# Kernel tuning notes

Hardware: AMD Instinct MI355X
Metric: run time of the kernel (lower is better)

Reference implementation:

```python
import jax, jax.numpy as jnp
import numpy as np

N_NODES = 50000
N_EDGES = 800000
N_TRAIN = 40000
IN_DIM = 129  # node_dim + encoding_dim


def _gatv2(x, src, dst, Wl, Wr, att, bias, heads, out_ch, n_nodes):
    """PyG GATv2Conv (share_weights=False, concat=True, aggr='mean', eval mode).
    x: [N, F_in]; src/dst: [E]; Wl/Wr: [F_in, heads*out_ch]; att: [heads, out_ch]."""
    xl = (x @ Wl).reshape(-1, heads, out_ch)          # source transform  [N,H,C]
    xr = (x @ Wr).reshape(-1, heads, out_ch)          # target transform  [N,H,C]
    e = jax.nn.leaky_relu(xl[src] + xr[dst], 0.2)     # [E,H,C]
    logits = jnp.einsum('ehc,hc->eh', e, att)         # [E,H]
    # segment softmax over incoming edges of each target node
    m = jax.ops.segment_max(logits, dst, num_segments=n_nodes)   # [N,H]
    a = jnp.exp(logits - m[dst])
    denom = jax.ops.segment_sum(a, dst, num_segments=n_nodes)    # [N,H]
    alpha = a / denom[dst]                                       # [E,H]
    msg = xl[src] * alpha[:, :, None]                            # [E,H,C]
    summed = jax.ops.segment_sum(msg, dst, num_segments=n_nodes) # [N,H,C]
    deg = jax.ops.segment_sum(jnp.ones((src.shape[0],), x.dtype), dst,
                              num_segments=n_nodes)              # aggr='mean'
    out = summed / jnp.maximum(deg, 1.0)[:, None, None]
    return out.reshape(n_nodes, heads * out_ch) + bias


def setup_inputs() -> dict:
    key = jax.random.key(0)
    ks = jax.random.split(key, 16)
    x = jax.random.normal(ks[0], (N_NODES, IN_DIM), jnp.float32)
    edge_index = jax.random.randint(ks[1], (2, N_EDGES), 0, N_NODES, jnp.int64)
    y = jax.random.uniform(ks[2], (N_NODES,), jnp.float32)
    train_idx = jnp.sort(jax.random.randint(ks[3], (N_TRAIN,), 0, N_NODES, jnp.int64))

    def lin(k, fi, fo):
        return jax.random.normal(k, (fi, fo), jnp.float32) * (1.0 / np.sqrt(fi))

    return {
        'x': x, 'edge_index': edge_index, 'y': y, 'train_idx': train_idx,
        # layer 1: 129 -> 128, heads=2 (concat -> 256)
        'W1l': lin(ks[4], IN_DIM, 256), 'W1r': lin(ks[5], IN_DIM, 256),
        'a1': jax.random.normal(ks[6], (2, 128), jnp.float32) * 0.1,
        'b1': jnp.zeros((256,), jnp.float32),
        # layer 2: 256 -> 128, heads=1
        'W2l': lin(ks[7], 256, 128), 'W2r': lin(ks[8], 256, 128),
        'a2': jax.random.normal(ks[9], (1, 128), jnp.float32) * 0.1,
        'b2': jnp.zeros((128,), jnp.float32),
        # layer 3: 128 -> 1, heads=1
        'W3l': lin(ks[10], 128, 1), 'W3r': lin(ks[11], 128, 1),
        'a3': jax.random.normal(ks[12], (1, 1), jnp.float32) * 0.1,
        'b3': jnp.zeros((1,), jnp.float32),
    }


def reference(x, edge_index, y, train_idx,
              W1l, W1r, a1, b1, W2l, W2r, a2, b2, W3l, W3r, a3, b3):
    src, dst = edge_index[0], edge_index[1]
    n = x.shape[0]
    h = _gatv2(x, src, dst, W1l, W1r, a1, b1, 2, 128, n)   # [N,256]
    h = _gatv2(h, src, dst, W2l, W2r, a2, b2, 1, 128, n)   # [N,128]
    h = _gatv2(h, src, dst, W3l, W3r, a3, b3, 1, 1, n)     # [N,1]
    pred = jax.nn.sigmoid(h.squeeze(-1))                   # [N]
    return pred[train_idx], y[train_idx]
```

## Files before the change

### kernel.cpp

```cpp
#include <hip/hip_runtime.h>
#include <cmath>

typedef __attribute__((ext_vector_type(2))) float v2f;

__device__ __forceinline__ float lo16(unsigned u){ union{unsigned x; float f;} c; c.x = u << 16; return c.f; }
__device__ __forceinline__ float hi16(unsigned u){ union{unsigned x; float f;} c; c.x = u & 0xffff0000u; return c.f; }
__device__ __forceinline__ float leaky(float v){ return fmaxf(v, 0.2f*v); }
__device__ __forceinline__ v2f pkmax(v2f a, v2f b){ v2f r; r.x = fmaxf(a.x,b.x); r.y = fmaxf(a.y,b.y); return r; }
__device__ __forceinline__ v2f mkv2(unsigned u){ v2f r; r.x = lo16(u); r.y = hi16(u); return r; }
__device__ __forceinline__ unsigned short f2bf(float f){
  union { float f; unsigned u; } c; c.f = f;
  unsigned u = c.u + 0x7FFFu + ((c.u >> 16) & 1u);
  return (unsigned short)(u >> 16);
}
__device__ __forceinline__ unsigned pack2bf(float a, float b){
  return (unsigned)f2bf(a) | ((unsigned)f2bf(b) << 16);
}
__device__ __forceinline__ float mergef(float m, float M){ return (m == M) ? 1.f : __expf(m - M); }

#define LOG2E 1.4426950408889634f

typedef __attribute__((ext_vector_type(8))) short bfrag;
typedef __attribute__((ext_vector_type(4))) float ffrag;


__global__ void deg_kernel(const int* __restrict__ dst, int* __restrict__ degi, int E){
  int e = blockIdx.x*256 + threadIdx.x;
  if (e < E) atomicAdd(&degi[dst[e]], 1);
}

__global__ void scan_p1(const int* __restrict__ degi, int* __restrict__ bsum, int N){
  __shared__ int red[256];
  int t = threadIdx.x;
  int i = blockIdx.x*256 + t;
  red[t] = (i < N) ? degi[i] : 0;
  __syncthreads();
  for (int off = 128; off > 0; off >>= 1){
    if (t < off) red[t] += red[t + off];
    __syncthreads();
  }
  if (t == 0) bsum[blockIdx.x] = red[0];
}

__global__ void scan_p2(const int* __restrict__ bsum, int* __restrict__ boff,
                        int* __restrict__ row_off, int NB, int N){
  __shared__ int s[256];
  int t = threadIdx.x;
  int v = (t < NB) ? bsum[t] : 0;
  s[t] = v;
  __syncthreads();
  for (int off = 1; off < 256; off <<= 1){
    int q = (t >= off) ? s[t - off] : 0;
    __syncthreads();
    s[t] += q;
    __syncthreads();
  }
  if (t < NB) boff[t] = s[t] - v;
  if (t == NB-1) row_off[N] = s[t];
}

__global__ void scan_p3(const int* __restrict__ degi, const int* __restrict__ boff,
                        int* __restrict__ row_off, int* __restrict__ cur, int N){
  __shared__ int s[256];
  int t = threadIdx.x;
  int i = blockIdx.x*256 + t;
  int v = (i < N) ? degi[i] : 0;
  s[t] = v;
  __syncthreads();
  for (int off = 1; off < 256; off <<= 1){
    int q = (t >= off) ? s[t - off] : 0;
    __syncthreads();
    s[t] += q;
    __syncthreads();
  }
  if (i < N){
    int ro = boff[blockIdx.x] + s[t] - v;
    row_off[i] = ro;
    cur[i] = ro;
  }
}

__global__ void scatter_kernel(const int* __restrict__ src, const int* __restrict__ dst,
                               int* __restrict__ cur, int* __restrict__ csr_src, int E){
  int e = blockIdx.x*256 + threadIdx.x;
  if (e < E){
    int pos = atomicAdd(&cur[dst[e]], 1);
    csr_src[pos] = src[e];
  }
}


__global__ void prep_all(const float* __restrict__ x,
                         const float* __restrict__ W1l, const float* __restrict__ W1r,
                         const float* __restrict__ W2l, const float* __restrict__ W2r,
                         unsigned short* __restrict__ Xbf,
                         unsigned short* __restrict__ WT1,
                         unsigned short* __restrict__ WT2, int N){
  int idx = blockIdx.x*256 + threadIdx.x;
  int n1 = N*160;
  int n2 = 2*256*160;
  int n3 = 2*128*256;
  if (idx < n1){
    int n = idx / 160, k = idx - n*160;
    Xbf[idx] = (k < 129) ? f2bf(x[(size_t)n*129 + k]) : (unsigned short)0;
  } else if (idx < n1 + n2){
    int j = idx - n1;
    int c = j / 160, k = j - c*160;
    float v = 0.f;
    if (k < 129) v = (c < 256) ? W1l[(size_t)k*256 + c] : W1r[(size_t)k*256 + (c - 256)];
    WT1[j] = f2bf(v);
  } else if (idx < n1 + n2 + n3){
    int j = idx - n1 - n2;
    int c = j >> 8, k = j & 255;
    float v = (c < 128) ? W2l[(size_t)k*128 + c] : W2r[(size_t)k*128 + (c - 128)];
    WT2[j] = f2bf(v);
  }
}


template<int CB>
__global__ __launch_bounds__(256) void gemm_dual(const unsigned short* __restrict__ Xbf,
                                                 const unsigned short* __restrict__ WT,
                                                 unsigned short* __restrict__ outL,
                                                 unsigned short* __restrict__ outR,
                                                 int N, int Kpad, int Mhalf){
  __shared__ __attribute__((aligned(16))) unsigned short Xs[128*40];
  __shared__ __attribute__((aligned(16))) unsigned short Ws[CB*128*40];
  int t = threadIdx.x;
  int n0 = blockIdx.x*128, c0 = blockIdx.y*(CB*128);
  int wv = t >> 6, lane = t & 63;
  int wr = wv >> 1, wc = wv & 1;
  int m16 = lane & 15, quad = lane >> 4;

  ffrag acc[CB][4][4];
  #pragma unroll
  for (int cb = 0; cb < CB; cb++)
    #pragma unroll
    for (int i = 0; i < 4; i++)
      #pragma unroll
      for (int j = 0; j < 4; j++) acc[cb][i][j] = (ffrag){0.f,0.f,0.f,0.f};

  for (int k0 = 0; k0 < Kpad; k0 += 32){
    uint4 zero = {0,0,0,0};
    #pragma unroll
    for (int it = 0; it < 2; it++){
      int idx = t + it*256;
      int r = idx >> 2, g = idx & 3;
      int n = n0 + r;
      uint4 v = (n < N) ? *(const uint4*)&Xbf[(size_t)n*Kpad + k0 + g*8] : zero;
      *(uint4*)&Xs[r*40 + g*8] = v;
    }
    #pragma unroll
    for (int it = 0; it < 2*CB; it++){
      int idx = t + it*256;
      int c = idx >> 2, g = idx & 3;
      uint4 v = *(const uint4*)&WT[(size_t)(c0 + c)*Kpad + k0 + g*8];
      *(uint4*)&Ws[c*40 + g*8] = v;
    }
    __syncthreads();
    bfrag a[4];
    #pragma unroll
    for (int i = 0; i < 4; i++)
      a[i] = *(const bfrag*)&Xs[(wr*64 + i*16 + m16)*40 + quad*8];
    #pragma unroll
    for (int cb = 0; cb < CB; cb++){
      bfrag b[4];
      #pragma unroll
      for (int j = 0; j < 4; j++)
        b[j] = *(const bfrag*)&Ws[(cb*128 + wc*64 + j*16 + m16)*40 + quad*8];
      #pragma unroll
      for (int i = 0; i < 4; i++)
        #pragma unroll
        for (int j = 0; j < 4; j++)
          acc[cb][i][j] = __builtin_amdgcn_mfma_f32_16x16x32_bf16(a[i], b[j], acc[cb][i][j], 0, 0, 0);
    }
    __syncthreads();
  }

  #pragma unroll
  for (int cb = 0; cb < CB; cb++){
    int gc0 = c0 + cb*128;
    bool isL = (gc0 < Mhalf);
    unsigned short* outp = isL ? outL : outR;
    int ccol0 = isL ? gc0 : (gc0 - Mhalf);
    #pragma unroll
    for (int i = 0; i < 4; i++){
      #pragma unroll
      for (int reg = 0; reg < 4; reg++){
        int rr = n0 + wr*64 + i*16 + quad*4 + reg;
        if (rr >= N) continue;
        #pragma unroll
        for (int j = 0; j < 4; j++){
          int cc = ccol0 + wc*64 + j*16 + m16;
          outp[(size_t)rr*Mhalf + cc] = f2bf(acc[cb][i][j][reg]);
        }
      }
    }
  }
}


__global__ __launch_bounds__(256) void fused_gat_wave2(
    const int* __restrict__ row_off, const int* __restrict__ csr_src,
    const unsigned short* __restrict__ xlbf, const unsigned short* __restrict__ xrbf,
    const float* __restrict__ att, const float* __restrict__ bias,
    unsigned short* __restrict__ outbf, int N)
{
  int n = blockIdx.x*4 + (threadIdx.x >> 6);
  if (n >= N) return;
  int lane = threadIdx.x & 63;
  int slot = lane >> 5;
  int sub  = lane & 31;
  int ch0  = sub*8;
  int r0 = row_off[n], r1 = row_off[n+1];
  int deg = r1 - r0;

  uint4 xru = *(const uint4*)&xrbf[(size_t)n*256 + ch0];
  v2f q01 = mkv2(xru.x), q23 = mkv2(xru.y), q45 = mkv2(xru.z), q67 = mkv2(xru.w);
  const v2f* atp = (const v2f*)(att + ch0);
  v2f at01 = atp[0], at23 = atp[1], at45 = atp[2], at67 = atp[3];

  float m = -INFINITY, l = 0.f;
  v2f A01 = {0.f,0.f}, A23 = {0.f,0.f}, A45 = {0.f,0.f}, A67 = {0.f,0.f};

  if (deg > 0){
    int p = r0 + slot;
    int pc = min(p, r1-1);
    uint4 cur = *(const uint4*)&xlbf[(size_t)csr_src[pc]*256 + ch0];
    for (; p < r1; p += 2){
      int pn = min(p+2, r1-1);
      uint4 nxt = *(const uint4*)&xlbf[(size_t)csr_src[pn]*256 + ch0];
      v2f x01 = mkv2(cur.x), x23 = mkv2(cur.y), x45 = mkv2(cur.z), x67 = mkv2(cur.w);
      v2f t01 = x01 + q01, t23 = x23 + q23, t45 = x45 + q45, t67 = x67 + q67;
      v2f dv = pkmax(t01, t01*0.2f)*at01;
      dv += pkmax(t23, t23*0.2f)*at23;
      dv += pkmax(t45, t45*0.2f)*at45;
      dv += pkmax(t67, t67*0.2f)*at67;
      float dot = dv.x + dv.y;
      dot += __shfl_xor(dot, 8);
      dot += __shfl_xor(dot, 4);
      dot += __shfl_xor(dot, 2);
      dot += __shfl_xor(dot, 1);
      if (dot <= m){
        float w_ = __expf(dot - m);
        l += w_;
        A01 += x01*w_; A23 += x23*w_; A45 += x45*w_; A67 += x67*w_;
      } else {
        float sc = __expf(m - dot);
        l = l*sc + 1.f;
        A01 = A01*sc + x01; A23 = A23*sc + x23; A45 = A45*sc + x45; A67 = A67*sc + x67;
        m = dot;
      }
      cur = nxt;
    }
  }

  const float4* bvp = (const float4*)(bias + ch0);
  float4 res0 = bvp[0], res1 = bvp[1];
  if (deg > 0){
    float m2 = __shfl_xor(m, 32);
    float l2 = __shfl_xor(l, 32);
    float M  = fmaxf(m, m2);
    float fa = mergef(m, M), fb = mergef(m2, M);
    float L  = l*fa + l2*fb;
    v2f q;
    q.x = __shfl_xor(A01.x,32); q.y = __shfl_xor(A01.y,32); A01 = A01*fa + q*fb;
    q.x = __shfl_xor(A23.x,32); q.y = __shfl_xor(A23.y,32); A23 = A23*fa + q*fb;
    q.x = __shfl_xor(A45.x,32); q.y = __shfl_xor(A45.y,32); A45 = A45*fa + q*fb;
    q.x = __shfl_xor(A67.x,32); q.y = __shfl_xor(A67.y,32); A67 = A67*fa + q*fb;
    float inv = 1.f / (L * (float)deg);
    res0.x += A01.x*inv; res0.y += A01.y*inv; res0.z += A23.x*inv; res0.w += A23.y*inv;
    res1.x += A45.x*inv; res1.y += A45.y*inv; res1.z += A67.x*inv; res1.w += A67.y*inv;
  }
  if (slot == 0){
    uint4 u;
    u.x = pack2bf(res0.x, res0.y);
    u.y = pack2bf(res0.z, res0.w);
    u.z = pack2bf(res1.x, res1.y);
    u.w = pack2bf(res1.z, res1.w);
    *(uint4*)&outbf[(size_t)n*256 + ch0] = u;
  }
}


__global__ __launch_bounds__(256) void fused_gat_wave1(
    const int* __restrict__ row_off, const int* __restrict__ csr_src,
    const unsigned short* __restrict__ xlbf, const unsigned short* __restrict__ xrbf,
    const float* __restrict__ att, const float* __restrict__ bias,
    const float* __restrict__ W3l, const float* __restrict__ W3r,
    float* __restrict__ xl3, float* __restrict__ xr3, int N)
{
  int n = blockIdx.x*4 + (threadIdx.x >> 6);
  if (n >= N) return;
  int lane = threadIdx.x & 63;
  int slot = lane >> 4;
  int sub  = lane & 15;
  int ch0  = sub*8;
  int r0 = row_off[n], r1 = row_off[n+1];
  int deg = r1 - r0;

  uint4 xru = *(const uint4*)&xrbf[(size_t)n*128 + ch0];
  v2f q01 = mkv2(xru.x), q23 = mkv2(xru.y), q45 = mkv2(xru.z), q67 = mkv2(xru.w);
  const v2f* atp = (const v2f*)(att + ch0);
  v2f at01 = atp[0], at23 = atp[1], at45 = atp[2], at67 = atp[3];

  float m = -INFINITY, l = 0.f;
  v2f A01 = {0.f,0.f}, A23 = {0.f,0.f}, A45 = {0.f,0.f}, A67 = {0.f,0.f};

  if (deg > 0){
    int p = r0 + slot;
    int pc = min(p, r1-1);
    uint4 cur = *(const uint4*)&xlbf[(size_t)csr_src[pc]*128 + ch0];
    for (; p < r1; p += 4){
      int pn = min(p+4, r1-1);
      uint4 nxt = *(const uint4*)&xlbf[(size_t)csr_src[pn]*128 + ch0];
      v2f x01 = mkv2(cur.x), x23 = mkv2(cur.y), x45 = mkv2(cur.z), x67 = mkv2(cur.w);
      v2f t01 = x01 + q01, t23 = x23 + q23, t45 = x45 + q45, t67 = x67 + q67;
      v2f dv = pkmax(t01, t01*0.2f)*at01;
      dv += pkmax(t23, t23*0.2f)*at23;
      dv += pkmax(t45, t45*0.2f)*at45;
      dv += pkmax(t67, t67*0.2f)*at67;
      float dot = dv.x + dv.y;
      dot += __shfl_xor(dot, 8);
      dot += __shfl_xor(dot, 4);
      dot += __shfl_xor(dot, 2);
      dot += __shfl_xor(dot, 1);
      if (dot <= m){
        float w_ = __expf(dot - m);
        l += w_;
        A01 += x01*w_; A23 += x23*w_; A45 += x45*w_; A67 += x67*w_;
      } else {
        float sc = __expf(m - dot);
        l = l*sc + 1.f;
        A01 = A01*sc + x01; A23 = A23*sc + x23; A45 = A45*sc + x45; A67 = A67*sc + x67;
        m = dot;
      }
      cur = nxt;
    }
  }

  if (deg > 0){
    #pragma unroll
    for (int stage = 0; stage < 2; stage++){
      int d = 16 << stage;
      float m2 = __shfl_xor(m, d);
      float l2 = __shfl_xor(l, d);
      float M  = fmaxf(m, m2);
      float fa = mergef(m, M), fb = mergef(m2, M);
      l = l*fa + l2*fb;
      v2f q;
      q.x = __shfl_xor(A01.x,d); q.y = __shfl_xor(A01.y,d); A01 = A01*fa + q*fb;
      q.x = __shfl_xor(A23.x,d); q.y = __shfl_xor(A23.y,d); A23 = A23*fa + q*fb;
      q.x = __shfl_xor(A45.x,d); q.y = __shfl_xor(A45.y,d); A45 = A45*fa + q*fb;
      q.x = __shfl_xor(A67.x,d); q.y = __shfl_xor(A67.y,d); A67 = A67*fa + q*fb;
      m = M;
    }
  }
  float inv = (deg > 0) ? 1.f/(l*(float)deg) : 0.f;
  const float4* bvp = (const float4*)(bias + ch0);
  float4 res0 = bvp[0], res1 = bvp[1];
  res0.x += A01.x*inv; res0.y += A01.y*inv; res0.z += A23.x*inv; res0.w += A23.y*inv;
  res1.x += A45.x*inv; res1.y += A45.y*inv; res1.z += A67.x*inv; res1.w += A67.y*inv;

  float4 wla = *(const float4*)(W3l + ch0);
  float4 wlb = *(const float4*)(W3l + ch0 + 4);
  float4 wra = *(const float4*)(W3r + ch0);
  float4 wrb = *(const float4*)(W3r + ch0 + 4);
  float sl = res0.x*wla.x + res0.y*wla.y + res0.z*wla.z + res0.w*wla.w
           + res1.x*wlb.x + res1.y*wlb.y + res1.z*wlb.z + res1.w*wlb.w;
  float sr = res0.x*wra.x + res0.y*wra.y + res0.z*wra.z + res0.w*wra.w
           + res1.x*wrb.x + res1.y*wrb.y + res1.z*wrb.z + res1.w*wrb.w;
  sl += __shfl_xor(sl, 8); sl += __shfl_xor(sl, 4); sl += __shfl_xor(sl, 2); sl += __shfl_xor(sl, 1);
  sr += __shfl_xor(sr, 8); sr += __shfl_xor(sr, 4); sr += __shfl_xor(sr, 2); sr += __shfl_xor(sr, 1);
  if (lane == 0){ xl3[n] = sl; xr3[n] = sr; }
}


__global__ __launch_bounds__(256) void aggr3_wave(
    const int* __restrict__ row_off, const int* __restrict__ csr_src,
    const float* __restrict__ xl3, const float* __restrict__ xr3,
    const float* __restrict__ a3, const float* __restrict__ b3,
    float* __restrict__ h3, int N)
{
  int n = blockIdx.x*4 + (threadIdx.x >> 6);
  if (n >= N) return;
  int lane = threadIdx.x & 63;
  int r0 = row_off[n], r1 = row_off[n+1];
  int deg = r1 - r0;
  float b = b3[0];
  if (deg == 0){ if (lane == 0) h3[n] = b; return; }
  float xrv = xr3[n];
  float aa = a3[0] * LOG2E;
  float m = -INFINITY, den = 0.f, s = 0.f;
  for (int base = r0; base < r1; base += 64){
    int p = base + lane;
    bool valid = p < r1;
    float xlv = valid ? xl3[csr_src[p]] : 0.f;
    float t = xlv + xrv;
    float v = fmaxf(t, 0.2f*t) * aa;
    if (!valid) v = -INFINITY;
    float bm = v;
    #pragma unroll
    for (int off = 32; off > 0; off >>= 1) bm = fmaxf(bm, __shfl_xor(bm, off));
    float nm = fmaxf(m, bm);
    float a = valid ? exp2f(v - nm) : 0.f;
    float bd = a, bs = a * xlv;
    #pragma unroll
    for (int off = 32; off > 0; off >>= 1){
      bd += __shfl_xor(bd, off);
      bs += __shfl_xor(bs, off);
    }
    float sc = exp2f(m - nm);
    den = den*sc + bd;
    s   = s*sc + bs;
    m = nm;
  }
  if (lane == 0) h3[n] = s/den/(float)deg + b;
}

__global__ void out_kernel(const float* __restrict__ h3, const float* __restrict__ y,
                           const int* __restrict__ tidx, float* __restrict__ out, int T){
  int i = blockIdx.x*256 + threadIdx.x;
  if (i >= T) return;
  int n = tidx[i];
  out[i] = 1.f/(1.f + __expf(-h3[n]));
  out[T + i] = y[n];
}


extern "C" void kernel_launch(void* const* d_in, const int* in_sizes, int n_in,
                              void* d_out, int out_size, void* d_ws, size_t ws_size,
                              hipStream_t stream){
  const float* x    = (const float*)d_in[0];
  const int*   ei   = (const int*)d_in[1];
  const float* y    = (const float*)d_in[2];
  const int*   tidx = (const int*)d_in[3];
  const float* W1l  = (const float*)d_in[4];
  const float* W1r  = (const float*)d_in[5];
  const float* a1   = (const float*)d_in[6];
  const float* b1   = (const float*)d_in[7];
  const float* W2l  = (const float*)d_in[8];
  const float* W2r  = (const float*)d_in[9];
  const float* a2   = (const float*)d_in[10];
  const float* b2   = (const float*)d_in[11];
  const float* W3l  = (const float*)d_in[12];
  const float* W3r  = (const float*)d_in[13];
  const float* a3   = (const float*)d_in[14];
  const float* b3   = (const float*)d_in[15];

  int N = in_sizes[2];
  int E = in_sizes[1] / 2;
  int T = in_sizes[3];
  const int* src = ei;
  const int* dst = ei + E;
  int NB = (N + 255) / 256;

  char* w = (char*)d_ws;
  size_t off = 0;
  auto take = [&](size_t bytes) -> char* {
    char* p = w + off;
    off = (off + bytes + 255) & ~(size_t)255;
    return p;
  };
  int*   row_off = (int*)  take((size_t)(N+1)*4);
  int*   degi    = (int*)  take((size_t)N*4);
  int*   cur     = (int*)  take((size_t)N*4);
  int*   bsum    = (int*)  take((size_t)NB*4);
  int*   boff    = (int*)  take((size_t)NB*4);
  int*   csr_src = (int*)  take((size_t)E*4);
  unsigned short* WT1 = (unsigned short*)take((size_t)512*160*2);
  unsigned short* WT2 = (unsigned short*)take((size_t)256*256*2);
  float* A       = (float*)take((size_t)N*256*4);
  float* B       = (float*)take((size_t)N*256*4);

  hipMemsetAsync(degi, 0, (size_t)N*4, stream);
  deg_kernel<<<(E+255)/256, 256, 0, stream>>>(dst, degi, E);
  scan_p1<<<NB, 256, 0, stream>>>(degi, bsum, N);
  scan_p2<<<1, 256, 0, stream>>>(bsum, boff, row_off, NB, N);
  scan_p3<<<NB, 256, 0, stream>>>(degi, boff, row_off, cur, N);
  scatter_kernel<<<(E+255)/256, 256, 0, stream>>>(src, dst, cur, csr_src, E);

  unsigned short* xl1bf = (unsigned short*)A;
  unsigned short* Xbf   = (unsigned short*)(A + (size_t)N*128);
  unsigned short* h1bf  = (unsigned short*)(A + (size_t)N*128);
  unsigned short* xr1bf = (unsigned short*)B;
  float* Bu   = B + (size_t)N*128;
  float* xl3  = Bu;
  float* xr3  = Bu + N;
  float* h3   = Bu + 2*(size_t)N;

  int prep_total = N*160 + 2*256*160 + 2*128*256;
  prep_all<<<(prep_total+255)/256, 256, 0, stream>>>(x, W1l, W1r, W2l, W2r, Xbf, WT1, WT2, N);

  gemm_dual<2><<<dim3((N+127)/128, 2), 256, 0, stream>>>(Xbf, WT1, xl1bf, xr1bf, N, 160, 256);
  fused_gat_wave2<<<(N+3)/4, 256, 0, stream>>>(row_off, csr_src, xl1bf, xr1bf, a1, b1, h1bf, N);

  unsigned short* xl2bf = (unsigned short*)A;
  unsigned short* xr2bf = (unsigned short*)B;
  gemm_dual<2><<<dim3((N+127)/128, 1), 256, 0, stream>>>(h1bf, WT2, xl2bf, xr2bf, N, 256, 128);
  fused_gat_wave1<<<(N+3)/4, 256, 0, stream>>>(row_off, csr_src, xl2bf, xr2bf, a2, b2,
                                               W3l, W3r, xl3, xr3, N);

  aggr3_wave<<<(N+3)/4, 256, 0, stream>>>(row_off, csr_src, xl3, xr3, a3, b3, h3, N);

  out_kernel<<<(T+255)/256, 256, 0, stream>>>(h3, y, tidx, (float*)d_out, T);
}
```

Baseline: 392.2 us.

## Merge CSR build and prep into one cooperative kernel; fuse layer-3 aggregation with output

Replaces the memset, degree count, three scan passes, scatter and input/weight conversion kernels with a single cooperative kernel that uses grid-wide syncs between phases. The final-layer aggregation now runs only for training-index nodes and writes the sigmoid and label output directly, which removes the separate output kernel and skips aggregation for nodes that are never read. This cuts launch count and per-launch gaps. In exchange, the CSR and prep phases run on a fixed 1024-block grid with grid barriers, which may lower parallelism compared with the original full-size launches.

```diff
diff --git a/kernel.cpp b/kernel.cpp
--- a/kernel.cpp
+++ b/kernel.cpp
@@ -1,11 +1,13 @@
 #include <hip/hip_runtime.h>
+#include <hip/hip_cooperative_groups.h>
 #include <cmath>
+
+namespace cg = cooperative_groups;
 
 typedef __attribute__((ext_vector_type(2))) float v2f;
 
 __device__ __forceinline__ float lo16(unsigned u){ union{unsigned x; float f;} c; c.x = u << 16; return c.f; }
 __device__ __forceinline__ float hi16(unsigned u){ union{unsigned x; float f;} c; c.x = u & 0xffff0000u; return c.f; }
-__device__ __forceinline__ float leaky(float v){ return fmaxf(v, 0.2f*v); }
 __device__ __forceinline__ v2f pkmax(v2f a, v2f b){ v2f r; r.x = fmaxf(a.x,b.x); r.y = fmaxf(a.y,b.y); return r; }
 __device__ __forceinline__ v2f mkv2(unsigned u){ v2f r; r.x = lo16(u); r.y = hi16(u); return r; }
 __device__ __forceinline__ unsigned short f2bf(float f){
@@ -24,96 +26,105 @@
 typedef __attribute__((ext_vector_type(4))) float ffrag;
 
 
-__global__ void deg_kernel(const int* __restrict__ dst, int* __restrict__ degi, int E){
-  int e = blockIdx.x*256 + threadIdx.x;
-  if (e < E) atomicAdd(&degi[dst[e]], 1);
-}
-
-__global__ void scan_p1(const int* __restrict__ degi, int* __restrict__ bsum, int N){
-  __shared__ int red[256];
-  int t = threadIdx.x;
-  int i = blockIdx.x*256 + t;
-  red[t] = (i < N) ? degi[i] : 0;
-  __syncthreads();
-  for (int off = 128; off > 0; off >>= 1){
-    if (t < off) red[t] += red[t + off];
-    __syncthreads();
-  }
-  if (t == 0) bsum[blockIdx.x] = red[0];
-}
-
-__global__ void scan_p2(const int* __restrict__ bsum, int* __restrict__ boff,
-                        int* __restrict__ row_off, int NB, int N){
+#define CSR_GRID 1024
+
+__global__ __launch_bounds__(256) void csr_prep_kernel(
+    const int* __restrict__ src, const int* __restrict__ dst,
+    int* __restrict__ degi, int* __restrict__ bsum, int* __restrict__ boff,
+    int* __restrict__ row_off, int* __restrict__ cur, int* __restrict__ csr_src,
+    const float* __restrict__ x,
+    const float* __restrict__ W1l, const float* __restrict__ W1r,
+    const float* __restrict__ W2l, const float* __restrict__ W2r,
+    unsigned short* __restrict__ Xbf, unsigned short* __restrict__ WT1,
+    unsigned short* __restrict__ WT2,
+    int N, int E, int NB)
+{
+  cg::grid_group grid = cg::this_grid();
   __shared__ int s[256];
   int t = threadIdx.x;
-  int v = (t < NB) ? bsum[t] : 0;
-  s[t] = v;
-  __syncthreads();
-  for (int off = 1; off < 256; off <<= 1){
-    int q = (t >= off) ? s[t - off] : 0;
-    __syncthreads();
-    s[t] += q;
-    __syncthreads();
-  }
-  if (t < NB) boff[t] = s[t] - v;
-  if (t == NB-1) row_off[N] = s[t];
-}
-
-__global__ void scan_p3(const int* __restrict__ degi, const int* __restrict__ boff,
-                        int* __restrict__ row_off, int* __restrict__ cur, int N){
-  __shared__ int s[256];
-  int t = threadIdx.x;
-  int i = blockIdx.x*256 + t;
-  int v = (i < N) ? degi[i] : 0;
-  s[t] = v;
-  __syncthreads();
-  for (int off = 1; off < 256; off <<= 1){
-    int q = (t >= off) ? s[t - off] : 0;
-    __syncthreads();
-    s[t] += q;
-    __syncthreads();
-  }
-  if (i < N){
-    int ro = boff[blockIdx.x] + s[t] - v;
-    row_off[i] = ro;
-    cur[i] = ro;
-  }
-}
-
-__global__ void scatter_kernel(const int* __restrict__ src, const int* __restrict__ dst,
-                               int* __restrict__ cur, int* __restrict__ csr_src, int E){
-  int e = blockIdx.x*256 + threadIdx.x;
-  if (e < E){
+  int gtid = blockIdx.x*256 + t;
+  int gsize = gridDim.x*256;
+
+  for (int i = gtid; i < N; i += gsize) degi[i] = 0;
+  {
+    int n1 = N*160;
+    int n2 = 2*256*160;
+    int n3 = 2*128*256;
+    int total = n1 + n2 + n3;
+    for (int idx = gtid; idx < total; idx += gsize){
+      if (idx < n1){
+        int n = idx / 160, k = idx - n*160;
+        Xbf[idx] = (k < 129) ? f2bf(x[(size_t)n*129 + k]) : (unsigned short)0;
+      } else if (idx < n1 + n2){
+        int j = idx - n1;
+        int c = j / 160, k = j - c*160;
+        float v = 0.f;
+        if (k < 129) v = (c < 256) ? W1l[(size_t)k*256 + c] : W1r[(size_t)k*256 + (c - 256)];
+        WT1[j] = f2bf(v);
+      } else {
+        int j = idx - n1 - n2;
+        int c = j >> 8, k = j & 255;
+        float v = (c < 128) ? W2l[(size_t)k*128 + c] : W2r[(size_t)k*128 + (c - 128)];
+        WT2[j] = f2bf(v);
+      }
+    }
+  }
+  grid.sync();
+
+  for (int e = gtid; e < E; e += gsize) atomicAdd(&degi[dst[e]], 1);
+  grid.sync();
+
+  for (int chunk = blockIdx.x; chunk < NB; chunk += gridDim.x){
+    int i = chunk*256 + t;
+    s[t] = (i < N) ? degi[i] : 0;
+    __syncthreads();
+    for (int off = 128; off > 0; off >>= 1){
+      if (t < off) s[t] += s[t + off];
+      __syncthreads();
+    }
+    if (t == 0) bsum[chunk] = s[0];
+    __syncthreads();
+  }
+  grid.sync();
+
+  if (blockIdx.x == 0){
+    int v = (t < NB) ? bsum[t] : 0;
+    s[t] = v;
+    __syncthreads();
+    for (int off = 1; off < 256; off <<= 1){
+      int q = (t >= off) ? s[t - off] : 0;
+      __syncthreads();
+      s[t] += q;
+      __syncthreads();
+    }
+    if (t < NB) boff[t] = s[t] - v;
+    if (t == NB-1) row_off[N] = s[t];
+  }
+  grid.sync();
+
+  for (int chunk = blockIdx.x; chunk < NB; chunk += gridDim.x){
+    int i = chunk*256 + t;
+    int v = (i < N) ? degi[i] : 0;
+    s[t] = v;
+    __syncthreads();
+    for (int off = 1; off < 256; off <<= 1){
+      int q = (t >= off) ? s[t - off] : 0;
+      __syncthreads();
+      s[t] += q;
+      __syncthreads();
+    }
+    if (i < N){
+      int ro = boff[chunk] + s[t] - v;
+      row_off[i] = ro;
+      cur[i] = ro;
+    }
+    __syncthreads();
+  }
+  grid.sync();
+
+  for (int e = gtid; e < E; e += gsize){
     int pos = atomicAdd(&cur[dst[e]], 1);
     csr_src[pos] = src[e];
-  }
-}
-
-
-__global__ void prep_all(const float* __restrict__ x,
-                         const float* __restrict__ W1l, const float* __restrict__ W1r,
-                         const float* __restrict__ W2l, const float* __restrict__ W2r,
-                         unsigned short* __restrict__ Xbf,
-                         unsigned short* __restrict__ WT1,
-                         unsigned short* __restrict__ WT2, int N){
-  int idx = blockIdx.x*256 + threadIdx.x;
-  int n1 = N*160;
-  int n2 = 2*256*160;
-  int n3 = 2*128*256;
-  if (idx < n1){
-    int n = idx / 160, k = idx - n*160;
-    Xbf[idx] = (k < 129) ? f2bf(x[(size_t)n*129 + k]) : (unsigned short)0;
-  } else if (idx < n1 + n2){
-    int j = idx - n1;
-    int c = j / 160, k = j - c*160;
-    float v = 0.f;
-    if (k < 129) v = (c < 256) ? W1l[(size_t)k*256 + c] : W1r[(size_t)k*256 + (c - 256)];
-    WT1[j] = f2bf(v);
-  } else if (idx < n1 + n2 + n3){
-    int j = idx - n1 - n2;
-    int c = j >> 8, k = j & 255;
-    float v = (c < 128) ? W2l[(size_t)k*128 + c] : W2r[(size_t)k*128 + (c - 128)];
-    WT2[j] = f2bf(v);
   }
 }
 
@@ -376,55 +387,56 @@
 }
 
 
-__global__ __launch_bounds__(256) void aggr3_wave(
+__global__ __launch_bounds__(256) void aggr3out_wave(
     const int* __restrict__ row_off, const int* __restrict__ csr_src,
     const float* __restrict__ xl3, const float* __restrict__ xr3,
     const float* __restrict__ a3, const float* __restrict__ b3,
-    float* __restrict__ h3, int N)
+    const float* __restrict__ y, const int* __restrict__ tidx,
+    float* __restrict__ out, int T)
 {
-  int n = blockIdx.x*4 + (threadIdx.x >> 6);
-  if (n >= N) return;
+  int i = blockIdx.x*4 + (threadIdx.x >> 6);
+  if (i >= T) return;
   int lane = threadIdx.x & 63;
+  int n = tidx[i];
   int r0 = row_off[n], r1 = row_off[n+1];
   int deg = r1 - r0;
   float b = b3[0];
-  if (deg == 0){ if (lane == 0) h3[n] = b; return; }
-  float xrv = xr3[n];
-  float aa = a3[0] * LOG2E;
-  float m = -INFINITY, den = 0.f, s = 0.f;
-  for (int base = r0; base < r1; base += 64){
-    int p = base + lane;
-    bool valid = p < r1;
-    float xlv = valid ? xl3[csr_src[p]] : 0.f;
-    float t = xlv + xrv;
-    float v = fmaxf(t, 0.2f*t) * aa;
-    if (!valid) v = -INFINITY;
-    float bm = v;
-    #pragma unroll
-    for (int off = 32; off > 0; off >>= 1) bm = fmaxf(bm, __shfl_xor(bm, off));
-    float nm = fmaxf(m, bm);
-    float a = valid ? exp2f(v - nm) : 0.f;
-    float bd = a, bs = a * xlv;
-    #pragma unroll
-    for (int off = 32; off > 0; off >>= 1){
-      bd += __shfl_xor(bd, off);
-      bs += __shfl_xor(bs, off);
-    }
-    float sc = exp2f(m - nm);
-    den = den*sc + bd;
-    s   = s*sc + bs;
-    m = nm;
-  }
-  if (lane == 0) h3[n] = s/den/(float)deg + b;
-}
-
-__global__ void out_kernel(const float* __restrict__ h3, const float* __restrict__ y,
-                           const int* __restrict__ tidx, float* __restrict__ out, int T){
-  int i = blockIdx.x*256 + threadIdx.x;
-  if (i >= T) return;
-  int n = tidx[i];
-  out[i] = 1.f/(1.f + __expf(-h3[n]));
-  out[T + i] = y[n];
+  float h;
+  if (deg == 0){
+    h = b;
+  } else {
+    float xrv = xr3[n];
+    float aa = a3[0] * LOG2E;
+    float m = -INFINITY, den = 0.f, s = 0.f;
+    for (int base = r0; base < r1; base += 64){
+      int p = base + lane;
+      bool valid = p < r1;
+      float xlv = valid ? xl3[csr_src[p]] : 0.f;
+      float t = xlv + xrv;
+      float v = fmaxf(t, 0.2f*t) * aa;
+      if (!valid) v = -INFINITY;
+      float bm = v;
+      #pragma unroll
+      for (int off = 32; off > 0; off >>= 1) bm = fmaxf(bm, __shfl_xor(bm, off));
+      float nm = fmaxf(m, bm);
+      float a = valid ? exp2f(v - nm) : 0.f;
+      float bd = a, bs = a * xlv;
+      #pragma unroll
+      for (int off = 32; off > 0; off >>= 1){
+        bd += __shfl_xor(bd, off);
+        bs += __shfl_xor(bs, off);
+      }
+      float sc = exp2f(m - nm);
+      den = den*sc + bd;
+      s   = s*sc + bs;
+      m = nm;
+    }
+    h = s/den/(float)deg + b;
+  }
+  if (lane == 0){
+    out[i] = 1.f/(1.f + __expf(-h));
+    out[T + i] = y[n];
+  }
 }
 
 
@@ -473,13 +485,6 @@
   float* A       = (float*)take((size_t)N*256*4);
   float* B       = (float*)take((size_t)N*256*4);
 
-  hipMemsetAsync(degi, 0, (size_t)N*4, stream);
-  deg_kernel<<<(E+255)/256, 256, 0, stream>>>(dst, degi, E);
-  scan_p1<<<NB, 256, 0, stream>>>(degi, bsum, N);
-  scan_p2<<<1, 256, 0, stream>>>(bsum, boff, row_off, NB, N);
-  scan_p3<<<NB, 256, 0, stream>>>(degi, boff, row_off, cur, N);
-  scatter_kernel<<<(E+255)/256, 256, 0, stream>>>(src, dst, cur, csr_src, E);
-
   unsigned short* xl1bf = (unsigned short*)A;
   unsigned short* Xbf   = (unsigned short*)(A + (size_t)N*128);
   unsigned short* h1bf  = (unsigned short*)(A + (size_t)N*128);
@@ -487,10 +492,18 @@
   float* Bu   = B + (size_t)N*128;
   float* xl3  = Bu;
   float* xr3  = Bu + N;
-  float* h3   = Bu + 2*(size_t)N;
-
-  int prep_total = N*160 + 2*256*160 + 2*128*256;
-  prep_all<<<(prep_total+255)/256, 256, 0, stream>>>(x, W1l, W1r, W2l, W2r, Xbf, WT1, WT2, N);
+
+  {
+    void* args[] = {
+      (void*)&src, (void*)&dst, (void*)&degi, (void*)&bsum, (void*)&boff,
+      (void*)&row_off, (void*)&cur, (void*)&csr_src,
+      (void*)&x, (void*)&W1l, (void*)&W1r, (void*)&W2l, (void*)&W2r,
+      (void*)&Xbf, (void*)&WT1, (void*)&WT2,
+      (void*)&N, (void*)&E, (void*)&NB
+    };
+    hipLaunchCooperativeKernel((const void*)csr_prep_kernel, dim3(CSR_GRID), dim3(256),
+                               args, 0, stream);
+  }
 
   gemm_dual<2><<<dim3((N+127)/128, 2), 256, 0, stream>>>(Xbf, WT1, xl1bf, xr1bf, N, 160, 256);
   fused_gat_wave2<<<(N+3)/4, 256, 0, stream>>>(row_off, csr_src, xl1bf, xr1bf, a1, b1, h1bf, N);
@@ -501,7 +514,6 @@
   fused_gat_wave1<<<(N+3)/4, 256, 0, stream>>>(row_off, csr_src, xl2bf, xr2bf, a2, b2,
                                                W3l, W3r, xl3, xr3, N);
 
-  aggr3_wave<<<(N+3)/4, 256, 0, stream>>>(row_off, csr_src, xl3, xr3, a3, b3, h3, N);
-
-  out_kernel<<<(T+255)/256, 256, 0, stream>>>(h3, y, tidx, (float*)d_out, T);
-}
+  aggr3out_wave<<<(T+3)/4, 256, 0, stream>>>(row_off, csr_src, xl3, xr3, a3, b3,
+                                             y, tidx, (float*)d_out, T);
+}
```

Result: slower. 979.0 us (+149.6%).
